# Optimization experiments

Measured on AMD Instinct MI355X. Metric: run time of the kernel, lower is better.

The kernel has to match this reference:

```python
import jax, jax.numpy as jnp
import numpy as np

NUM_CHANNELS = 512
B_DIM = 64
C_DIM = 16
N = 512
FEAT = NUM_CHANNELS * 4 * 4  # 8192


def setup_inputs() -> dict:
    key = jax.random.key(0)
    k1, k2 = jax.random.split(key)
    inp = jax.random.normal(k1, (N, NUM_CHANNELS, 4, 4), dtype=jnp.float32)
    T = jax.random.normal(k2, (FEAT, B_DIM * C_DIM), dtype=jnp.float32) * 0.1
    return {"inp": inp, "T": T}


def reference(inp, T):
    x = inp.reshape(-1, FEAT)                      # (N, 8192)
    M = (x @ T).reshape(-1, B_DIM, C_DIM)          # (N, B, C)
    # pairwise L1 distance over C: (N, N, B)
    dist = jnp.sum(jnp.abs(M[:, None, :, :] - M[None, :, :, :]), axis=-1)
    o = jnp.sum(jnp.exp(-dist), axis=1)            # (N, B)
    return jnp.concatenate((x, o), axis=1)         # (N, 8192 + B)
```

## Files before the change

kernel.cpp:

```cpp
#include <hip/hip_runtime.h>

#define NROWS 512
#define FEAT  8192
#define BDIM  64
#define CDIM  16
#define MCOLS 1024
#define OUTC  8256
#define KSPLIT 8
#define KCHUNK (FEAT / KSPLIT)
#define KSTEPS (KCHUNK / 64)
#define MSIZE  (NROWS * MCOLS)

typedef __bf16 bf16x8 __attribute__((ext_vector_type(8)));
typedef float  floatx4 __attribute__((ext_vector_type(4)));

static __device__ __forceinline__ unsigned int pk2(float a, float b) {
    unsigned short lo = __builtin_bit_cast(unsigned short, (__bf16)a);
    unsigned short hi = __builtin_bit_cast(unsigned short, (__bf16)b);
    return (unsigned int)lo | ((unsigned int)hi << 16);
}

__global__ __launch_bounds__(512, 2) void k_gemm(const float* __restrict__ x,
                                                 const float* __restrict__ T,
                                                 float* __restrict__ Mp,
                                                 float* __restrict__ out) {
    __shared__ __align__(16) unsigned short ldsA[2][128 * 64];
    __shared__ __align__(16) unsigned short ldsB[2][128 * 64];
    char* ldsAc = (char*)ldsA;
    char* ldsBc = (char*)ldsB;

    int bid = blockIdx.x;
    int wg = (bid & 7) * 32 + (bid >> 3);
    int mt = wg & 3, nt = (wg >> 2) & 7, ks = wg >> 5;
    int m0 = mt * 128, n0 = nt * 128, kbase = ks * KCHUNK;
    int t = threadIdx.x, w = t >> 6, l = t & 63;
    bool docopy = (nt == ks);

    int arow = t >> 4, aq = t & 15;
    const float* gA = x + (size_t)(m0 + arow) * FEAT + kbase + aq * 4;
    float* gC = out + (size_t)(m0 + arow) * OUTC + kbase + aq * 4;
    int swa = (arow & 7) ^ ((arow >> 2) & 7);
    int wA = arow * 128 + (((aq >> 1) ^ swa) << 4) + ((aq & 1) << 3);

    int n4 = t & 31, kg = t >> 5;
    const float* gB = T + (size_t)(kbase + kg * 4) * MCOLS + n0 + n4 * 4;
    int wB0, wB1, wB2, wB3;
    {
        int n_0 = n4 * 4 + 0, n_1 = n4 * 4 + 1, n_2 = n4 * 4 + 2, n_3 = n4 * 4 + 3;
        wB0 = n_0 * 128 + (((kg >> 1) ^ ((n_0 & 7) ^ ((n_0 >> 2) & 7))) << 4) + ((kg & 1) << 3);
        wB1 = n_1 * 128 + (((kg >> 1) ^ ((n_1 & 7) ^ ((n_1 >> 2) & 7))) << 4) + ((kg & 1) << 3);
        wB2 = n_2 * 128 + (((kg >> 1) ^ ((n_2 & 7) ^ ((n_2 >> 2) & 7))) << 4) + ((kg & 1) << 3);
        wB3 = n_3 * 128 + (((kg >> 1) ^ ((n_3 & 7) ^ ((n_3 >> 2) & 7))) << 4) + ((kg & 1) << 3);
    }

    int wr = w >> 2, wc = w & 3, fm = l & 15, fq = l >> 4;
    int swf = (fm & 7) ^ ((fm >> 2) & 7);
    int baseA = (wr * 64 + fm) * 128 + ((fq ^ swf) << 4);
    int baseB = (wc * 32 + fm) * 128 + ((fq ^ swf) << 4);

    floatx4 acc[4][2] = {};

    float4 va00, va01, va02, va03, vb00, vb01, vb02, vb03;
    float4 va10, va11, va12, va13, vb10, vb11, vb12, vb13;

#define ISSUE(A0, A1, A2, A3, B0, B1, B2, B3, KK) do {                      \
        const float* pa_ = gA + (KK) * 64;                                  \
        A0 = *(const float4*)(pa_);                                         \
        A1 = *(const float4*)(pa_ + 32 * FEAT);                             \
        A2 = *(const float4*)(pa_ + 64 * FEAT);                             \
        A3 = *(const float4*)(pa_ + 96 * FEAT);                             \
        const float* pb_ = gB + (size_t)(KK) * 64 * MCOLS;                  \
        B0 = *(const float4*)(pb_);                                         \
        B1 = *(const float4*)(pb_ + MCOLS);                                 \
        B2 = *(const float4*)(pb_ + 2 * MCOLS);                             \
        B3 = *(const float4*)(pb_ + 3 * MCOLS);                             \
    } while (0)

#define KEEP(A0, A1, A2, A3, B0, B1, B2, B3)                                \
    asm volatile("" ::                                                      \
        "v"(A0.x), "v"(A0.y), "v"(A0.z), "v"(A0.w),                         \
        "v"(A1.x), "v"(A1.y), "v"(A1.z), "v"(A1.w),                         \
        "v"(A2.x), "v"(A2.y), "v"(A2.z), "v"(A2.w),                         \
        "v"(A3.x), "v"(A3.y), "v"(A3.z), "v"(A3.w),                         \
        "v"(B0.x), "v"(B0.y), "v"(B0.z), "v"(B0.w),                         \
        "v"(B1.x), "v"(B1.y), "v"(B1.z), "v"(B1.w),                         \
        "v"(B2.x), "v"(B2.y), "v"(B2.z), "v"(B2.w),                         \
        "v"(B3.x), "v"(B3.y), "v"(B3.z), "v"(B3.w))

#define WRITE(A0, A1, A2, A3, B0, B1, B2, B3, SO, KK) do {                  \
        uint2 u_;                                                           \
        u_.x = pk2(A0.x, A0.y); u_.y = pk2(A0.z, A0.w);                     \
        *(uint2*)(ldsAc + (SO) + wA + 0 * 4096) = u_;                       \
        u_.x = pk2(A1.x, A1.y); u_.y = pk2(A1.z, A1.w);                     \
        *(uint2*)(ldsAc + (SO) + wA + 1 * 4096) = u_;                       \
        u_.x = pk2(A2.x, A2.y); u_.y = pk2(A2.z, A2.w);                     \
        *(uint2*)(ldsAc + (SO) + wA + 2 * 4096) = u_;                       \
        u_.x = pk2(A3.x, A3.y); u_.y = pk2(A3.z, A3.w);                     \
        *(uint2*)(ldsAc + (SO) + wA + 3 * 4096) = u_;                       \
        u_.x = pk2(B0.x, B1.x); u_.y = pk2(B2.x, B3.x);                     \
        *(uint2*)(ldsBc + (SO) + wB0) = u_;                                 \
        u_.x = pk2(B0.y, B1.y); u_.y = pk2(B2.y, B3.y);                     \
        *(uint2*)(ldsBc + (SO) + wB1) = u_;                                 \
        u_.x = pk2(B0.z, B1.z); u_.y = pk2(B2.z, B3.z);                     \
        *(uint2*)(ldsBc + (SO) + wB2) = u_;                                 \
        u_.x = pk2(B0.w, B1.w); u_.y = pk2(B2.w, B3.w);                     \
        *(uint2*)(ldsBc + (SO) + wB3) = u_;                                 \
        if (docopy) {                                                       \
            *(float4*)(gC + (size_t)0 * 32 * OUTC + (KK) * 64) = A0;        \
            *(float4*)(gC + (size_t)1 * 32 * OUTC + (KK) * 64) = A1;        \
            *(float4*)(gC + (size_t)2 * 32 * OUTC + (KK) * 64) = A2;        \
            *(float4*)(gC + (size_t)3 * 32 * OUTC + (KK) * 64) = A3;        \
        }                                                                   \
    } while (0)

#define MFMA_PHASE(SO) do {                                                 \
        _Pragma("unroll")                                                   \
        for (int h = 0; h < 2; ++h) {                                       \
            bf16x8 af[4], bfr[2];                                           \
            _Pragma("unroll")                                               \
            for (int a = 0; a < 4; ++a)                                     \
                af[a] = *(const bf16x8*)(ldsAc + (SO) + ((baseA + a * 2048) ^ ((h ^ (a & 1)) << 6))); \
            _Pragma("unroll")                                               \
            for (int b = 0; b < 2; ++b)                                     \
                bfr[b] = *(const bf16x8*)(ldsBc + (SO) + ((baseB + b * 2048) ^ ((h ^ (b & 1)) << 6))); \
            _Pragma("unroll")                                               \
            for (int a = 0; a < 4; ++a)                                     \
                _Pragma("unroll")                                           \
                for (int b = 0; b < 2; ++b)                                 \
                    acc[a][b] = __builtin_amdgcn_mfma_f32_16x16x32_bf16(af[a], bfr[b], acc[a][b], 0, 0, 0); \
        }                                                                   \
    } while (0)

    ISSUE(va00, va01, va02, va03, vb00, vb01, vb02, vb03, 0);
    ISSUE(va10, va11, va12, va13, vb10, vb11, vb12, vb13, 1);
    for (int kk = 0; kk < KSTEPS; kk += 2) {
        WRITE(va00, va01, va02, va03, vb00, vb01, vb02, vb03, 0, kk);
        if (kk + 2 < KSTEPS)
            ISSUE(va00, va01, va02, va03, vb00, vb01, vb02, vb03, kk + 2);
        asm volatile("s_waitcnt lgkmcnt(0)" ::: "memory");
        __builtin_amdgcn_sched_barrier(0);
        __builtin_amdgcn_s_barrier();
        MFMA_PHASE(0);
        KEEP(va10, va11, va12, va13, vb10, vb11, vb12, vb13);
        WRITE(va10, va11, va12, va13, vb10, vb11, vb12, vb13, 16384, kk + 1);
        if (kk + 3 < KSTEPS)
            ISSUE(va10, va11, va12, va13, vb10, vb11, vb12, vb13, kk + 3);
        asm volatile("s_waitcnt lgkmcnt(0)" ::: "memory");
        __builtin_amdgcn_sched_barrier(0);
        __builtin_amdgcn_s_barrier();
        MFMA_PHASE(16384);
        KEEP(va00, va01, va02, va03, vb00, vb01, vb02, vb03);
    }
#undef ISSUE
#undef KEEP
#undef WRITE
#undef MFMA_PHASE

    float* outp = Mp + (size_t)ks * MSIZE;
    int b0 = nt * 8 + wc * 2;
    int gr0 = m0 + wr * 64;
#pragma unroll
    for (int a = 0; a < 4; ++a)
#pragma unroll
        for (int r = 0; r < 4; ++r) {
            int row = gr0 + a * 16 + fq * 4 + r;
#pragma unroll
            for (int b = 0; b < 2; ++b)
                outp[(size_t)(b0 + b) * (NROWS * CDIM) + row * CDIM + fm] = acc[a][b][r];
        }
}

__global__ __launch_bounds__(512, 1) void k_pair(const float* __restrict__ Mp,
                                                 float* __restrict__ out) {
    __shared__ __align__(16) float ldsM[NROWS * CDIM];
    __shared__ float partial[8][64];
    int bid = blockIdx.x, t = threadIdx.x;
    int b = bid & 63, itp = bid >> 6;
    const float* slab = Mp + (size_t)b * (NROWS * CDIM);

#pragma unroll
    for (int p = 0; p < 4; ++p) {
        int idx = t + p * 512;
        float4 s = *(const float4*)(slab + (size_t)idx * 4);
#pragma unroll
        for (int k = 1; k < KSPLIT; ++k) {
            float4 v = *(const float4*)(slab + (size_t)k * MSIZE + (size_t)idx * 4);
            s.x += v.x; s.y += v.y; s.z += v.z; s.w += v.w;
        }
        *(float4*)&ldsM[idx * 4] = s;
    }
    __syncthreads();

    int lane = t & 63, w = t >> 6, g = t >> 8, wg = (t >> 6) & 3;
    int i = (itp * 2 + g) * 64 + lane;
    float4 mi0 = *(const float4*)&ldsM[i * CDIM + 0];
    float4 mi1 = *(const float4*)&ldsM[i * CDIM + 4];
    float4 mi2 = *(const float4*)&ldsM[i * CDIM + 8];
    float4 mi3 = *(const float4*)&ldsM[i * CDIM + 12];

    float acc = 0.0f;
    for (int jj = wg * 128; jj < wg * 128 + 128; ++jj) {
        const float4* rp = (const float4*)&ldsM[jj * CDIM];
        float4 a0 = rp[0], a1 = rp[1], a2 = rp[2], a3 = rp[3];
        float d = fabsf(mi0.x - a0.x) + fabsf(mi0.y - a0.y)
                + fabsf(mi0.z - a0.z) + fabsf(mi0.w - a0.w)
                + fabsf(mi1.x - a1.x) + fabsf(mi1.y - a1.y)
                + fabsf(mi1.z - a1.z) + fabsf(mi1.w - a1.w)
                + fabsf(mi2.x - a2.x) + fabsf(mi2.y - a2.y)
                + fabsf(mi2.z - a2.z) + fabsf(mi2.w - a2.w)
                + fabsf(mi3.x - a3.x) + fabsf(mi3.y - a3.y)
                + fabsf(mi3.z - a3.z) + fabsf(mi3.w - a3.w);
        acc += __expf(-d);
    }
    partial[w][lane] = acc;
    __syncthreads();
    if ((t & 255) < 64) {
        int ii = (itp * 2 + g) * 64 + (t & 63);
        float o = partial[g * 4 + 0][t & 63] + partial[g * 4 + 1][t & 63] +
                  partial[g * 4 + 2][t & 63] + partial[g * 4 + 3][t & 63];
        out[(size_t)ii * OUTC + FEAT + b] = o;
    }
}

extern "C" void kernel_launch(void* const* d_in, const int* in_sizes, int n_in,
                              void* d_out, int out_size, void* d_ws, size_t ws_size,
                              hipStream_t stream) {
    const float* x = (const float*)d_in[0];
    const float* T = (const float*)d_in[1];
    float* out = (float*)d_out;

    float* Mp = (float*)d_ws;

    k_gemm<<<256, 512, 0, stream>>>(x, T, Mp, out);
    k_pair<<<256, 512, 0, stream>>>(Mp, out);
}
```

Before: 125.3 us.

## Add prep kernel converting x and transposed T to bf16 before GEMM

```diff
diff --git a/kernel.cpp b/kernel.cpp
--- a/kernel.cpp
+++ b/kernel.cpp
@@ -14,16 +14,60 @@
 typedef __bf16 bf16x8 __attribute__((ext_vector_type(8)));
 typedef float  floatx4 __attribute__((ext_vector_type(4)));
 
-static __device__ __forceinline__ unsigned int pk2(float a, float b) {
-    unsigned short lo = __builtin_bit_cast(unsigned short, (__bf16)a);
-    unsigned short hi = __builtin_bit_cast(unsigned short, (__bf16)b);
-    return (unsigned int)lo | ((unsigned int)hi << 16);
-}
-
-__global__ __launch_bounds__(512, 2) void k_gemm(const float* __restrict__ x,
+static __device__ __forceinline__ unsigned short f2bf(float f) {
+    unsigned int x = __builtin_bit_cast(unsigned int, f);
+    unsigned int r = (x + 0x7FFFu + ((x >> 16) & 1u)) >> 16;
+    return (unsigned short)r;
+}
+
+__global__ __launch_bounds__(512, 2) void k_prep(const float* __restrict__ x,
                                                  const float* __restrict__ T,
-                                                 float* __restrict__ Mp,
+                                                 unsigned short* __restrict__ xb,
+                                                 unsigned short* __restrict__ Tt,
                                                  float* __restrict__ out) {
+    __shared__ __align__(16) float lds[2][64][65];
+    int bid = blockIdx.x, t = threadIdx.x;
+#pragma unroll
+    for (int u = 0; u < 8; ++u) {
+        int gid = bid * 4096 + u * 512 + t;
+        float4 v = *(const float4*)(x + (size_t)gid * 4);
+        ushort4 uu;
+        uu.x = f2bf(v.x); uu.y = f2bf(v.y); uu.z = f2bf(v.z); uu.w = f2bf(v.w);
+        *(ushort4*)(xb + (size_t)gid * 4) = uu;
+        int row = gid >> 11, col4 = gid & 2047;
+        *(float4*)(out + (size_t)row * OUTC + col4 * 4) = v;
+    }
+    int sub = t >> 8, tt = t & 255;
+    for (int u = 0; u < 4; ++u) {
+        int tile = bid * 8 + u * 2 + sub;
+        int kt = tile & 127, nt = tile >> 7;
+        __syncthreads();
+        int kk = tt >> 2, q = tt & 3;
+#pragma unroll
+        for (int p = 0; p < 4; ++p) {
+            int c4 = q + p * 4;
+            float4 v = *(const float4*)(T + (size_t)(kt * 64 + kk) * MCOLS + nt * 64 + c4 * 4);
+            lds[sub][kk][c4 * 4 + 0] = v.x; lds[sub][kk][c4 * 4 + 1] = v.y;
+            lds[sub][kk][c4 * 4 + 2] = v.z; lds[sub][kk][c4 * 4 + 3] = v.w;
+        }
+        __syncthreads();
+        int nr = tt >> 2, ck = tt & 3;
+        unsigned int wv[8];
+#pragma unroll
+        for (int j = 0; j < 8; ++j) {
+            unsigned int lo = f2bf(lds[sub][ck * 16 + j * 2 + 0][nr]);
+            unsigned int hi = f2bf(lds[sub][ck * 16 + j * 2 + 1][nr]);
+            wv[j] = lo | (hi << 16);
+        }
+        uint4* dst = (uint4*)(Tt + (size_t)(nt * 64 + nr) * FEAT + kt * 64 + ck * 16);
+        dst[0] = make_uint4(wv[0], wv[1], wv[2], wv[3]);
+        dst[1] = make_uint4(wv[4], wv[5], wv[6], wv[7]);
+    }
+}
+
+__global__ __launch_bounds__(512, 2) void k_gemm(const unsigned short* __restrict__ xb,
+                                                 const unsigned short* __restrict__ Tt,
+                                                 float* __restrict__ Mp) {
     __shared__ __align__(16) unsigned short ldsA[2][128 * 64];
     __shared__ __align__(16) unsigned short ldsB[2][128 * 64];
     char* ldsAc = (char*)ldsA;
@@ -34,24 +78,13 @@
     int mt = wg & 3, nt = (wg >> 2) & 7, ks = wg >> 5;
     int m0 = mt * 128, n0 = nt * 128, kbase = ks * KCHUNK;
     int t = threadIdx.x, w = t >> 6, l = t & 63;
-    bool docopy = (nt == ks);
-
-    int arow = t >> 4, aq = t & 15;
-    const float* gA = x + (size_t)(m0 + arow) * FEAT + kbase + aq * 4;
-    float* gC = out + (size_t)(m0 + arow) * OUTC + kbase + aq * 4;
-    int swa = (arow & 7) ^ ((arow >> 2) & 7);
-    int wA = arow * 128 + (((aq >> 1) ^ swa) << 4) + ((aq & 1) << 3);
-
-    int n4 = t & 31, kg = t >> 5;
-    const float* gB = T + (size_t)(kbase + kg * 4) * MCOLS + n0 + n4 * 4;
-    int wB0, wB1, wB2, wB3;
-    {
-        int n_0 = n4 * 4 + 0, n_1 = n4 * 4 + 1, n_2 = n4 * 4 + 2, n_3 = n4 * 4 + 3;
-        wB0 = n_0 * 128 + (((kg >> 1) ^ ((n_0 & 7) ^ ((n_0 >> 2) & 7))) << 4) + ((kg & 1) << 3);
-        wB1 = n_1 * 128 + (((kg >> 1) ^ ((n_1 & 7) ^ ((n_1 >> 2) & 7))) << 4) + ((kg & 1) << 3);
-        wB2 = n_2 * 128 + (((kg >> 1) ^ ((n_2 & 7) ^ ((n_2 >> 2) & 7))) << 4) + ((kg & 1) << 3);
-        wB3 = n_3 * 128 + (((kg >> 1) ^ ((n_3 & 7) ^ ((n_3 >> 2) & 7))) << 4) + ((kg & 1) << 3);
-    }
+
+    int srow = t >> 2, c = t & 3;
+    const unsigned short* gA = xb + (size_t)(m0 + srow) * FEAT + kbase + c * 8;
+    const unsigned short* gB = Tt + (size_t)(n0 + srow) * FEAT + kbase + c * 8;
+    int sws = (srow & 7) ^ ((srow >> 2) & 7);
+    int wS1 = srow * 128 + ((c ^ sws) << 4);
+    int wS2 = wS1 ^ 64;
 
     int wr = w >> 2, wc = w & 3, fm = l & 15, fq = l >> 4;
     int swf = (fm & 7) ^ ((fm >> 2) & 7);
@@ -60,57 +93,30 @@
 
     floatx4 acc[4][2] = {};
 
-    float4 va00, va01, va02, va03, vb00, vb01, vb02, vb03;
-    float4 va10, va11, va12, va13, vb10, vb11, vb12, vb13;
-
-#define ISSUE(A0, A1, A2, A3, B0, B1, B2, B3, KK) do {                      \
-        const float* pa_ = gA + (KK) * 64;                                  \
-        A0 = *(const float4*)(pa_);                                         \
-        A1 = *(const float4*)(pa_ + 32 * FEAT);                             \
-        A2 = *(const float4*)(pa_ + 64 * FEAT);                             \
-        A3 = *(const float4*)(pa_ + 96 * FEAT);                             \
-        const float* pb_ = gB + (size_t)(KK) * 64 * MCOLS;                  \
-        B0 = *(const float4*)(pb_);                                         \
-        B1 = *(const float4*)(pb_ + MCOLS);                                 \
-        B2 = *(const float4*)(pb_ + 2 * MCOLS);                             \
-        B3 = *(const float4*)(pb_ + 3 * MCOLS);                             \
+    uint4 a01, a02, b01, b02;
+    uint4 a11, a12, b11, b12;
+
+#define ISSUE(A1, A2, B1, B2, KK) do {                                      \
+        const unsigned short* pa_ = gA + (KK) * 64;                         \
+        A1 = *(const uint4*)(pa_);                                          \
+        A2 = *(const uint4*)(pa_ + 32);                                     \
+        const unsigned short* pb_ = gB + (KK) * 64;                         \
+        B1 = *(const uint4*)(pb_);                                          \
+        B2 = *(const uint4*)(pb_ + 32);                                     \
     } while (0)
 
-#define KEEP(A0, A1, A2, A3, B0, B1, B2, B3)                                \
+#define KEEP(A1, A2, B1, B2)                                                \
     asm volatile("" ::                                                      \
-        "v"(A0.x), "v"(A0.y), "v"(A0.z), "v"(A0.w),                         \
         "v"(A1.x), "v"(A1.y), "v"(A1.z), "v"(A1.w),                         \
         "v"(A2.x), "v"(A2.y), "v"(A2.z), "v"(A2.w),                         \
-        "v"(A3.x), "v"(A3.y), "v"(A3.z), "v"(A3.w),                         \
-        "v"(B0.x), "v"(B0.y), "v"(B0.z), "v"(B0.w),                         \
         "v"(B1.x), "v"(B1.y), "v"(B1.z), "v"(B1.w),                         \
-        "v"(B2.x), "v"(B2.y), "v"(B2.z), "v"(B2.w),                         \
-        "v"(B3.x), "v"(B3.y), "v"(B3.z), "v"(B3.w))
-
-#define WRITE(A0, A1, A2, A3, B0, B1, B2, B3, SO, KK) do {                  \
-        uint2 u_;                                                           \
-        u_.x = pk2(A0.x, A0.y); u_.y = pk2(A0.z, A0.w);                     \
-        *(uint2*)(ldsAc + (SO) + wA + 0 * 4096) = u_;                       \
-        u_.x = pk2(A1.x, A1.y); u_.y = pk2(A1.z, A1.w);                     \
-        *(uint2*)(ldsAc + (SO) + wA + 1 * 4096) = u_;                       \
-        u_.x = pk2(A2.x, A2.y); u_.y = pk2(A2.z, A2.w);                     \
-        *(uint2*)(ldsAc + (SO) + wA + 2 * 4096) = u_;                       \
-        u_.x = pk2(A3.x, A3.y); u_.y = pk2(A3.z, A3.w);                     \
-        *(uint2*)(ldsAc + (SO) + wA + 3 * 4096) = u_;                       \
-        u_.x = pk2(B0.x, B1.x); u_.y = pk2(B2.x, B3.x);                     \
-        *(uint2*)(ldsBc + (SO) + wB0) = u_;                                 \
-        u_.x = pk2(B0.y, B1.y); u_.y = pk2(B2.y, B3.y);                     \
-        *(uint2*)(ldsBc + (SO) + wB1) = u_;                                 \
-        u_.x = pk2(B0.z, B1.z); u_.y = pk2(B2.z, B3.z);                     \
-        *(uint2*)(ldsBc + (SO) + wB2) = u_;                                 \
-        u_.x = pk2(B0.w, B1.w); u_.y = pk2(B2.w, B3.w);                     \
-        *(uint2*)(ldsBc + (SO) + wB3) = u_;                                 \
-        if (docopy) {                                                       \
-            *(float4*)(gC + (size_t)0 * 32 * OUTC + (KK) * 64) = A0;        \
-            *(float4*)(gC + (size_t)1 * 32 * OUTC + (KK) * 64) = A1;        \
-            *(float4*)(gC + (size_t)2 * 32 * OUTC + (KK) * 64) = A2;        \
-            *(float4*)(gC + (size_t)3 * 32 * OUTC + (KK) * 64) = A3;        \
-        }                                                                   \
+        "v"(B2.x), "v"(B2.y), "v"(B2.z), "v"(B2.w))
+
+#define WRITE(A1, A2, B1, B2, SO) do {                                      \
+        *(uint4*)(ldsAc + (SO) + wS1) = A1;                                 \
+        *(uint4*)(ldsAc + (SO) + wS2) = A2;                                 \
+        *(uint4*)(ldsBc + (SO) + wS1) = B1;                                 \
+        *(uint4*)(ldsBc + (SO) + wS2) = B2;                                 \
     } while (0)
 
 #define MFMA_PHASE(SO) do {                                                 \
@@ -131,25 +137,23 @@
         }                                                                   \
     } while (0)
 
-    ISSUE(va00, va01, va02, va03, vb00, vb01, vb02, vb03, 0);
-    ISSUE(va10, va11, va12, va13, vb10, vb11, vb12, vb13, 1);
+    ISSUE(a01, a02, b01, b02, 0);
+    ISSUE(a11, a12, b11, b12, 1);
     for (int kk = 0; kk < KSTEPS; kk += 2) {
-        WRITE(va00, va01, va02, va03, vb00, vb01, vb02, vb03, 0, kk);
-        if (kk + 2 < KSTEPS)
-            ISSUE(va00, va01, va02, va03, vb00, vb01, vb02, vb03, kk + 2);
+        WRITE(a01, a02, b01, b02, 0);
+        if (kk + 2 < KSTEPS) ISSUE(a01, a02, b01, b02, kk + 2);
         asm volatile("s_waitcnt lgkmcnt(0)" ::: "memory");
         __builtin_amdgcn_sched_barrier(0);
         __builtin_amdgcn_s_barrier();
         MFMA_PHASE(0);
-        KEEP(va10, va11, va12, va13, vb10, vb11, vb12, vb13);
-        WRITE(va10, va11, va12, va13, vb10, vb11, vb12, vb13, 16384, kk + 1);
-        if (kk + 3 < KSTEPS)
-            ISSUE(va10, va11, va12, va13, vb10, vb11, vb12, vb13, kk + 3);
+        KEEP(a11, a12, b11, b12);
+        WRITE(a11, a12, b11, b12, 16384);
+        if (kk + 3 < KSTEPS) ISSUE(a11, a12, b11, b12, kk + 3);
         asm volatile("s_waitcnt lgkmcnt(0)" ::: "memory");
         __builtin_amdgcn_sched_barrier(0);
         __builtin_amdgcn_s_barrier();
         MFMA_PHASE(16384);
-        KEEP(va00, va01, va02, va03, vb00, vb01, vb02, vb03);
+        KEEP(a01, a02, b01, b02);
     }
 #undef ISSUE
 #undef KEEP
@@ -229,8 +233,11 @@
     const float* T = (const float*)d_in[1];
     float* out = (float*)d_out;
 
-    float* Mp = (float*)d_ws;
-
-    k_gemm<<<256, 512, 0, stream>>>(x, T, Mp, out);
+    unsigned short* xb = (unsigned short*)d_ws;
+    unsigned short* Tt = (unsigned short*)((char*)d_ws + (8u << 20));
+    float*          Mp = (float*)((char*)d_ws + (24u << 20));
+
+    k_prep<<<256, 512, 0, stream>>>(x, T, xb, Tt, out);
+    k_gemm<<<256, 512, 0, stream>>>(xb, Tt, Mp);
     k_pair<<<256, 512, 0, stream>>>(Mp, out);
 }
```

Result: no change. 127.3 us (+1.6%).

## Fuse split-K reduction into GEMM via last-block atomic counter

Applied to the files above, without the earlier changes.

```diff
diff --git a/kernel.cpp b/kernel.cpp
--- a/kernel.cpp
+++ b/kernel.cpp
@@ -23,9 +23,12 @@
 __global__ __launch_bounds__(512, 2) void k_gemm(const float* __restrict__ x,
                                                  const float* __restrict__ T,
                                                  float* __restrict__ Mp,
+                                                 float* __restrict__ Mfin,
+                                                 int* __restrict__ flags,
                                                  float* __restrict__ out) {
     __shared__ __align__(16) unsigned short ldsA[2][128 * 64];
     __shared__ __align__(16) unsigned short ldsB[2][128 * 64];
+    __shared__ int lastFlag;
     char* ldsAc = (char*)ldsA;
     char* ldsBc = (char*)ldsB;
 
@@ -168,25 +171,42 @@
             for (int b = 0; b < 2; ++b)
                 outp[(size_t)(b0 + b) * (NROWS * CDIM) + row * CDIM + fm] = acc[a][b][r];
         }
-}
-
-__global__ __launch_bounds__(512, 1) void k_pair(const float* __restrict__ Mp,
+
+    __threadfence();
+    __syncthreads();
+    if (t == 0) lastFlag = atomicAdd(&flags[wg & 31], 1);
+    __syncthreads();
+    if (lastFlag == KSPLIT - 1) {
+        __threadfence();
+        int br = nt * 8;
+#pragma unroll
+        for (int u = 0; u < 8; ++u) {
+            int pos = u * 2048 + t * 4;
+            int bi = pos >> 11, inner = pos & 2047;
+            size_t off = (size_t)(br + bi) * (NROWS * CDIM) + (size_t)m0 * CDIM + inner;
+            float4 s = *(const float4*)(Mp + off);
+#pragma unroll
+            for (int k2 = 1; k2 < KSPLIT; ++k2) {
+                float4 v = *(const float4*)(Mp + (size_t)k2 * MSIZE + off);
+                s.x += v.x; s.y += v.y; s.z += v.z; s.w += v.w;
+            }
+            *(float4*)(Mfin + off) = s;
+        }
+    }
+}
+
+__global__ __launch_bounds__(512, 1) void k_pair(const float* __restrict__ Mfin,
                                                  float* __restrict__ out) {
     __shared__ __align__(16) float ldsM[NROWS * CDIM];
     __shared__ float partial[8][64];
     int bid = blockIdx.x, t = threadIdx.x;
     int b = bid & 63, itp = bid >> 6;
-    const float* slab = Mp + (size_t)b * (NROWS * CDIM);
+    const float* slab = Mfin + (size_t)b * (NROWS * CDIM);
 
 #pragma unroll
     for (int p = 0; p < 4; ++p) {
         int idx = t + p * 512;
         float4 s = *(const float4*)(slab + (size_t)idx * 4);
-#pragma unroll
-        for (int k = 1; k < KSPLIT; ++k) {
-            float4 v = *(const float4*)(slab + (size_t)k * MSIZE + (size_t)idx * 4);
-            s.x += v.x; s.y += v.y; s.z += v.z; s.w += v.w;
-        }
         *(float4*)&ldsM[idx * 4] = s;
     }
     __syncthreads();
@@ -229,8 +249,11 @@
     const float* T = (const float*)d_in[1];
     float* out = (float*)d_out;
 
-    float* Mp = (float*)d_ws;
-
-    k_gemm<<<256, 512, 0, stream>>>(x, T, Mp, out);
-    k_pair<<<256, 512, 0, stream>>>(Mp, out);
-}
+    float* Mp   = (float*)d_ws;
+    float* Mfin = (float*)((char*)d_ws + (16u << 20));
+    int*   flags = (int*)((char*)d_ws + (18u << 20));
+
+    hipMemsetAsync(flags, 0, 32 * sizeof(int), stream);
+    k_gemm<<<256, 512, 0, stream>>>(x, T, Mp, Mfin, flags, out);
+    k_pair<<<256, 512, 0, stream>>>(Mfin, out);
+}
```

After: 214.1 us. +70.9%, slower.
